# Performance work log

Measured on AMD Instinct MI355X. Metric: run time of the kernel, lower is better.

## Reference

```python
import jax, jax.numpy as jnp
import numpy as np

# ---- config (from repo's config module, standard values) ----
GH, GW = 32, 64            # control grid
FULL_H, FULL_W = 128, 512  # target_image (n_mels, frames)
N_FFT, HOP = 1024, 256
N_FREQ = N_FFT // 2 + 1    # 513
N_ITER, MOMENTUM = 32, 0.99
NUM_SAMPLES = 131072
BATCH = 8

# periodic hann window (torch.hann_window default)
_WIN = 0.5 * (1.0 - jnp.cos(2.0 * jnp.pi * jnp.arange(N_FFT) / N_FFT))


def _stft(x):
    # x: (B, L) -> (B, N_FREQ, F); center=True reflect pad, hann window
    pad = N_FFT // 2
    xp = jnp.pad(x, ((0, 0), (pad, pad)), mode='reflect')
    n_frames = 1 + (xp.shape[-1] - N_FFT) // HOP
    idx = jnp.arange(n_frames)[:, None] * HOP + jnp.arange(N_FFT)[None, :]
    frames = xp[:, idx] * _WIN  # (B, F, N_FFT)
    return jnp.fft.rfft(frames, axis=-1).transpose(0, 2, 1)  # (B, N_FREQ, F)


def _istft(S, length):
    # S: (B, N_FREQ, F) -> (B, length); windowed overlap-add, center trim
    frames = jnp.fft.irfft(S.transpose(0, 2, 1), n=N_FFT, axis=-1) * _WIN  # (B,F,N_FFT)
    B, F, _ = frames.shape
    total = N_FFT + HOP * (F - 1)
    idx = (jnp.arange(F)[:, None] * HOP + jnp.arange(N_FFT)[None, :]).reshape(-1)
    sig = jnp.zeros((B, total), frames.dtype).at[:, idx].add(frames.reshape(B, -1))
    wsq = jnp.zeros((total,), frames.dtype).at[idx].add(jnp.tile(_WIN ** 2, F))
    sig = sig / jnp.where(wsq > 1e-11, wsq, 1.0)
    pad = N_FFT // 2
    return sig[:, pad:pad + length]


def _griffin_lim(spec_power):
    # spec_power: (B, N_FREQ, W) power spectrogram (power=2.0)
    mag = jnp.sqrt(jnp.maximum(spec_power, 0.0))
    W = spec_power.shape[-1]
    length = HOP * (W - 1)
    # random unit-magnitude initial phase (torchaudio rand_init)
    u = jax.random.uniform(jax.random.key(1), mag.shape, dtype=jnp.float32)
    angles = jnp.exp(1j * (2.0 * jnp.pi) * u).astype(jnp.complex64)
    tprev = jnp.zeros_like(angles)
    for _ in range(N_ITER):  # fixed 32 iterations
        inverse = _istft(mag.astype(jnp.complex64) * angles, length)
        rebuilt = _stft(inverse)
        angles = rebuilt - tprev * (MOMENTUM / (1.0 + MOMENTUM))
        angles = angles / (jnp.abs(angles) + 1e-16)
        tprev = rebuilt
    return _istft(mag.astype(jnp.complex64) * angles, length)  # (B, length)


def setup_inputs() -> dict:
    key = jax.random.key(0)
    params = jax.random.uniform(key, (BATCH, GH * GW), dtype=jnp.float32)
    return {"params": params}


def reference(params):
    B = params.shape[0]
    grid = params.reshape(B, GH, GW)
    # F.interpolate(..., mode='bilinear', align_corners=False) == jax.image.resize bilinear
    full_spec = jax.image.resize(grid, (B, FULL_H, FULL_W), method='bilinear')  # (B,H,W)
    spec_power = full_spec ** 2 * 100.0
    linear_spec = jax.image.resize(spec_power, (B, N_FREQ, FULL_W), method='bilinear')
    audio = _griffin_lim(linear_spec)  # (B, (W-1)*HOP)
    # pad/trim to NUM_SAMPLES
    L = audio.shape[-1]
    if L < NUM_SAMPLES:
        audio = jnp.pad(audio, ((0, 0), (0, NUM_SAMPLES - L)))
    else:
        audio = audio[:, :NUM_SAMPLES]
    max_val = jnp.maximum(jnp.max(jnp.abs(audio), axis=-1, keepdims=True), 1e-8)
    audio = audio / max_val * 0.9
    return audio, full_spec
```

## Files before the change

kernel.cpp:

```cpp
#include <hip/hip_runtime.h>

typedef unsigned int u32;

constexpr int BATCH = 8;
constexpr int GH = 32, GW = 64;
constexpr int FH = 128, FW = 512;
constexpr int NFFT = 1024;
constexpr int HOP = 256;
constexpr int NFREQ = 513;
constexpr int NW = 512;
constexpr int SIGLEN = HOP * (NW - 1);
constexpr int TOTAL_LEN = NFFT + HOP*(NW-1);
constexpr int NITER = 32;
constexpr int NSAMP = 131072;
constexpr int NMAG = BATCH * NW * NFREQ;

#define SL(i) ((i) + ((i) >> 3))
constexpr int WSL = 576;

#define WAVEFENCE() __builtin_amdgcn_wave_barrier()

__device__ __forceinline__ void tf_round(u32 &x0, u32 &x1, int r) {
  x0 += x1;
  x1 = (x1 << r) | (x1 >> (32 - r));
  x1 ^= x0;
}

__device__ __forceinline__ void threefry2(u32 c0, u32 c1, u32 &o0, u32 &o1) {
  const u32 k0 = 0u, k1 = 1u;
  const u32 k2 = 0x1BD11BDAu ^ k0 ^ k1;
  u32 x0 = c0 + k0, x1 = c1 + k1;
  tf_round(x0, x1, 13); tf_round(x0, x1, 15); tf_round(x0, x1, 26); tf_round(x0, x1, 6);
  x0 += k1; x1 += k2 + 1u;
  tf_round(x0, x1, 17); tf_round(x0, x1, 29); tf_round(x0, x1, 16); tf_round(x0, x1, 24);
  x0 += k2; x1 += k0 + 2u;
  tf_round(x0, x1, 13); tf_round(x0, x1, 15); tf_round(x0, x1, 26); tf_round(x0, x1, 6);
  x0 += k0; x1 += k1 + 3u;
  tf_round(x0, x1, 17); tf_round(x0, x1, 29); tf_round(x0, x1, 16); tf_round(x0, x1, 24);
  x0 += k1; x1 += k2 + 4u;
  tf_round(x0, x1, 13); tf_round(x0, x1, 15); tf_round(x0, x1, 26); tf_round(x0, x1, 6);
  x0 += k2; x1 += k0 + 5u;
  o0 = x0; o1 = x1;
}

__global__ __launch_bounds__(256) void k_init(float* __restrict__ win,
                                              float2* __restrict__ tw512f, double2* __restrict__ twh,
                                              float* __restrict__ wsq,
                                              float2* __restrict__ tprev)
{
  int idx = blockIdx.x * 256 + threadIdx.x;
  int stride = gridDim.x * 256;
  const double PI2 = 6.283185307179586476925286766559;
  for (int t = idx; t < NFFT; t += stride)
    win[t] = (float)(0.5 * (1.0 - cos(PI2 * (double)t / 1024.0)));
  for (int k = idx; k < 512; k += stride) {
    double th = -PI2 * (double)k / 512.0;
    tw512f[k] = make_float2((float)cos(th), (float)sin(th));
    double th2 = -PI2 * (double)k / 1024.0;
    double2 v2; v2.x = cos(th2); v2.y = sin(th2);
    twh[k] = v2;
  }
  for (int j = idx; j < TOTAL_LEN; j += stride) {
    int gmax = j >> 8; if (gmax > NW - 1) gmax = NW - 1;
    int gmin = (j >= NFFT) ? ((j - (NFFT - 1) + 255) >> 8) : 0;
    float acc = 0.f;
    for (int g = gmin; g <= gmax; ++g) {
      float w = (float)(0.5 * (1.0 - cos(PI2 * (double)(j - (g << 8)) / 1024.0)));
      acc = __fadd_rn(acc, __fmul_rn(w, w));
    }
    wsq[j] = acc;
  }
  for (int i = idx; i < NMAG; i += stride)
    tprev[i] = make_float2(0.f, 0.f);
}

__device__ __forceinline__ void lin_taps(float sf, int in, int &i0, int &i1, float &w0, float &w1)
{
  if (sf <= 0.0f)                  { i0 = 0;      i1 = 0;      w0 = 1.0f; w1 = 0.0f; return; }
  if (sf >= (float)(in - 1))       { i0 = in - 1; i1 = in - 1; w0 = 1.0f; w1 = 0.0f; return; }
  i0 = (int)sf; i1 = i0 + 1;
  float x0 = __fsub_rn(sf, (float)i0);
  float a0 = __fsub_rn(1.0f, x0);
  float S  = __fadd_rn(a0, x0);
  w0 = __fdiv_rn(a0, S);
  w1 = __fdiv_rn(x0, S);
}

__device__ __forceinline__ float sf_H1(int H) {
  return __fadd_rn(__fmul_rn(__fadd_rn((float)H, 0.5f), 0.25f), -0.5f);
}
__device__ __forceinline__ float sf_W1(int W) {
  return __fadd_rn(__fmul_rn(__fadd_rn((float)W, 0.5f), 0.125f), -0.5f);
}
__device__ __forceinline__ float sf_H2(int K) {
  const float inv32 = (float)(1.0 / 4.0078125);
  return __fadd_rn(__fmul_rn(__fadd_rn((float)K, 0.5f), inv32), -0.5f);
}

__device__ __forceinline__ float fs_at(const float* __restrict__ pb, int H, int W)
{
  int r0, r1; float u0, u1;
  lin_taps(sf_H1(H), GH, r0, r1, u0, u1);
  int c0, c1; float v0, v1;
  lin_taps(sf_W1(W), GW, c0, c1, v0, v1);
  float t0 = __fmaf_rn(u1, pb[r1 * GW + c0], __fmul_rn(u0, pb[r0 * GW + c0]));
  float t1 = __fmaf_rn(u1, pb[r1 * GW + c1], __fmul_rn(u0, pb[r0 * GW + c1]));
  return __fmaf_rn(v1, t1, __fmul_rn(v0, t0));
}

__global__ __launch_bounds__(256) void k_fullspec(const float* __restrict__ p, float* __restrict__ fs)
{
  int idx = blockIdx.x * 256 + threadIdx.x;
  if (idx >= BATCH * FH * FW) return;
  int b = idx >> 16;
  int h = (idx >> 9) & (FH - 1);
  int w = idx & (FW - 1);
  fs[idx] = fs_at(p + b * (GH * GW), h, w);
}

__global__ __launch_bounds__(256) void k_mag(const float* __restrict__ p, float* __restrict__ mag)
{
  int idx = blockIdx.x * 256 + threadIdx.x;
  if (idx >= NMAG) return;
  int b = idx / (NW * NFREQ);
  int rem = idx - b * (NW * NFREQ);
  int f = rem / NFREQ;
  int k = rem - f * NFREQ;
  const float* pb = p + b * (GH * GW);
  int h0, h1; float wa, wb;
  lin_taps(sf_H2(k), FH, h0, h1, wa, wb);
  float fs0 = fs_at(pb, h0, f);
  float fs1 = fs_at(pb, h1, f);
  float P0 = __fmul_rn(__fmul_rn(fs0, fs0), 100.0f);
  float P1 = __fmul_rn(__fmul_rn(fs1, fs1), 100.0f);
  float lin = __fmaf_rn(wb, P1, __fmul_rn(wa, P0));
  mag[idx] = __fsqrt_rn(fmaxf(lin, 0.0f));
}

__global__ __launch_bounds__(256) void k_phase(float2* __restrict__ ang)
{
  int idx = blockIdx.x * 256 + threadIdx.x;
  if (idx >= NMAG) return;
  int b = idx / (NW * NFREQ);
  int rem = idx - b * (NW * NFREQ);
  int f = rem / NFREQ;
  int k = rem - f * NFREQ;
  u32 cnt = (u32)(b * (NFREQ * NW) + k * NW + f);
  u32 w0, w1;
  threefry2(0u, cnt, w0, w1);
  u32 bits = w0 ^ w1;
  float u = __uint_as_float((bits >> 9) | 0x3f800000u) - 1.0f;
  float th = __fmul_rn((float)6.283185307179586, u);
  double thd = (double)th;
  ang[idx] = make_float2((float)cos(thd), (float)sin(thd));
}

__device__ __forceinline__ float2 cadd2(float2 a, float2 b){ return make_float2(a.x+b.x, a.y+b.y); }
__device__ __forceinline__ float2 csub2(float2 a, float2 b){ return make_float2(a.x-b.x, a.y-b.y); }

template<bool INV>
__device__ __forceinline__ float2 twmul(float2 a, float2 w)
{
  float wy = INV ? -w.y : w.y;
  return make_float2(a.x*w.x - a.y*wy, a.x*wy + a.y*w.x);
}

template<bool INV>
__device__ __forceinline__ void bfly8(float2 x0, float2 x1, float2 x2, float2 x3,
                                      float2 x4, float2 x5, float2 x6, float2 x7,
                                      float2 &Y0, float2 &Y1, float2 &Y2, float2 &Y3,
                                      float2 &Y4, float2 &Y5, float2 &Y6, float2 &Y7)
{
  const float c = 0.70710678118654752440f;
  float2 u0 = cadd2(x0,x4), u1 = cadd2(x1,x5), u2 = cadd2(x2,x6), u3 = cadd2(x3,x7);
  float2 d0 = csub2(x0,x4), d1 = csub2(x1,x5), d2 = csub2(x2,x6), d3 = csub2(x3,x7);
  float2 w1, w2, w3;
  if (!INV) {
    w1 = make_float2(c*(d1.x + d1.y), c*(d1.y - d1.x));
    w2 = make_float2(d2.y, -d2.x);
    w3 = make_float2(c*(d3.y - d3.x), -c*(d3.x + d3.y));
  } else {
    w1 = make_float2(c*(d1.x - d1.y), c*(d1.x + d1.y));
    w2 = make_float2(-d2.y, d2.x);
    w3 = make_float2(-c*(d3.x + d3.y), c*(d3.x - d3.y));
  }
  float2 s0 = cadd2(u0,u2), s1 = cadd2(u1,u3), s2 = csub2(u0,u2);
  float2 e13 = csub2(u1,u3);
  float2 s3 = INV ? make_float2(-e13.y, e13.x) : make_float2(e13.y, -e13.x);
  float2 r0 = cadd2(d0,w2), r1 = cadd2(w1,w3), r2 = csub2(d0,w2);
  float2 e57 = csub2(w1,w3);
  float2 r3 = INV ? make_float2(-e57.y, e57.x) : make_float2(e57.y, -e57.x);
  Y0 = cadd2(s0,s1); Y4 = csub2(s0,s1);
  Y2 = cadd2(s2,s3); Y6 = csub2(s2,s3);
  Y1 = cadd2(r0,r1); Y5 = csub2(r0,r1);
  Y3 = cadd2(r2,r3); Y7 = csub2(r2,r3);
}

template<bool INV>
__device__ __forceinline__ void stage0_regs(float2* __restrict__ A, const float2* __restrict__ tw, int t,
    float2 x0, float2 x1, float2 x2, float2 x3, float2 x4, float2 x5, float2 x6, float2 x7)
{
  float2 Y0,Y1,Y2,Y3,Y4,Y5,Y6,Y7;
  bfly8<INV>(x0,x1,x2,x3,x4,x5,x6,x7, Y0,Y1,Y2,Y3,Y4,Y5,Y6,Y7);
  int ob = 8 * t;
  A[SL(ob + 0)] = Y0;
  A[SL(ob + 1)] = twmul<INV>(Y1, tw[t]);
  A[SL(ob + 2)] = twmul<INV>(Y2, tw[2 * t]);
  A[SL(ob + 3)] = twmul<INV>(Y3, tw[3 * t]);
  A[SL(ob + 4)] = twmul<INV>(Y4, tw[4 * t]);
  A[SL(ob + 5)] = twmul<INV>(Y5, tw[5 * t]);
  A[SL(ob + 6)] = twmul<INV>(Y6, tw[6 * t]);
  A[SL(ob + 7)] = twmul<INV>(Y7, tw[7 * t]);
}

template<bool INV>
__device__ __forceinline__ void stage_mid(float2* __restrict__ A, const float2* __restrict__ tw, int t)
{
  float2 x0 = A[SL(t)],       x1 = A[SL(t + 64)],  x2 = A[SL(t + 128)], x3 = A[SL(t + 192)];
  float2 x4 = A[SL(t + 256)], x5 = A[SL(t + 320)], x6 = A[SL(t + 384)], x7 = A[SL(t + 448)];
  float2 Y0,Y1,Y2,Y3,Y4,Y5,Y6,Y7;
  bfly8<INV>(x0,x1,x2,x3,x4,x5,x6,x7, Y0,Y1,Y2,Y3,Y4,Y5,Y6,Y7);
  WAVEFENCE();
  int p = t >> 3, q = t & 7;
  int base = 8 * p;
  int ob = q + 64 * p;
  A[SL(ob)]      = Y0;
  A[SL(ob + 8)]  = twmul<INV>(Y1, tw[base]);
  A[SL(ob + 16)] = twmul<INV>(Y2, tw[2 * base]);
  A[SL(ob + 24)] = twmul<INV>(Y3, tw[3 * base]);
  A[SL(ob + 32)] = twmul<INV>(Y4, tw[4 * base]);
  A[SL(ob + 40)] = twmul<INV>(Y5, tw[5 * base]);
  A[SL(ob + 48)] = twmul<INV>(Y6, tw[6 * base]);
  A[SL(ob + 56)] = twmul<INV>(Y7, tw[7 * base]);
}

template<bool INV>
__device__ __forceinline__ void stage_last_lds(float2* __restrict__ A, int t)
{
  float2 x0 = A[SL(t)],       x1 = A[SL(t + 64)],  x2 = A[SL(t + 128)], x3 = A[SL(t + 192)];
  float2 x4 = A[SL(t + 256)], x5 = A[SL(t + 320)], x6 = A[SL(t + 384)], x7 = A[SL(t + 448)];
  float2 Y0,Y1,Y2,Y3,Y4,Y5,Y6,Y7;
  bfly8<INV>(x0,x1,x2,x3,x4,x5,x6,x7, Y0,Y1,Y2,Y3,Y4,Y5,Y6,Y7);
  WAVEFENCE();
  A[SL(t)]       = Y0; A[SL(t + 64)]  = Y1; A[SL(t + 128)] = Y2; A[SL(t + 192)] = Y3;
  A[SL(t + 256)] = Y4; A[SL(t + 320)] = Y5; A[SL(t + 384)] = Y6; A[SL(t + 448)] = Y7;
}

template<bool INV>
__device__ __forceinline__ void stage_last_regs(const float2* __restrict__ A, int t,
    float2 &Y0, float2 &Y1, float2 &Y2, float2 &Y3, float2 &Y4, float2 &Y5, float2 &Y6, float2 &Y7)
{
  float2 x0 = A[SL(t)],       x1 = A[SL(t + 64)],  x2 = A[SL(t + 128)], x3 = A[SL(t + 192)];
  float2 x4 = A[SL(t + 256)], x5 = A[SL(t + 320)], x6 = A[SL(t + 384)], x7 = A[SL(t + 448)];
  bfly8<INV>(x0,x1,x2,x3,x4,x5,x6,x7, Y0,Y1,Y2,Y3,Y4,Y5,Y6,Y7);
}

__device__ __forceinline__ void upd_bin(float2* __restrict__ prow, float2* __restrict__ A,
                                        int k, double rx, double ry, float cf)
{
  float rxf = (float)rx, ryf = (float)ry;
  float2 pv = prow[k];
  float ax = __fsub_rn(rxf, __fmul_rn(pv.x, cf));
  float ay = __fsub_rn(ryf, __fmul_rn(pv.y, cf));
  double dx = (double)ax, dy = (double)ay;
  float d = (float)sqrt(dx * dx + dy * dy);
  float d2 = __fadd_rn(d, 1e-16f);
  float inv = __fdiv_rn(1.0f, d2);
  int slot = (k == 512) ? (WSL - 1) : SL(k);
  A[slot] = make_float2(__fmul_rn(ax, inv), __fmul_rn(ay, inv));
  prow[k] = make_float2(rxf, ryf);
}

__global__ __launch_bounds__(256) void k_istft(const float* __restrict__ mag, const float2* __restrict__ ang,
                                               float* __restrict__ frames,
                                               const float2* __restrict__ tw512f,
                                               const double2* __restrict__ twh,
                                               const float* __restrict__ win)
{
  __shared__ float2 ldsA[4 * WSL];
  __shared__ float2 twl[512];
  int tid = threadIdx.x;
  for (int i = tid; i < 512; i += 256) twl[i] = tw512f[i];
  __syncthreads();

  int wv = tid >> 6;
  int t  = tid & 63;
  int bf = (blockIdx.x << 2) + wv;
  float2* A = ldsA + wv * WSL;
  const float*  mrow = mag + bf * NFREQ;
  const float2* arow = ang + bf * NFREQ;

  float2 z0, z1, z2, z3, z4, z5, z6, z7;
#define PACKG(j, zj) { \
    int k = t + 64 * j; \
    if (k == 0) { \
      float m1 = mrow[0];   float2 a1 = arow[0]; \
      float m2 = mrow[512]; float2 a2 = arow[512]; \
      float S1x = __fmul_rn(m1, a1.x); \
      float S2x = __fmul_rn(m2, a2.x); \
      zj = make_float2((float)(0.5 * ((double)S1x + (double)S2x)), \
                       (float)(0.5 * ((double)S1x - (double)S2x))); \
    } else { \
      int k2 = 512 - k; \
      float m1 = mrow[k];  float2 a1 = arow[k]; \
      float m2 = mrow[k2]; float2 a2 = arow[k2]; \
      float S1x = __fmul_rn(m1, a1.x), S1y = __fmul_rn(m1, a1.y); \
      float S2x = __fmul_rn(m2, a2.x), S2y = __fmul_rn(m2, a2.y); \
      double Xex = 0.5 * ((double)S1x + (double)S2x); \
      double Xey = 0.5 * ((double)S1y - (double)S2y); \
      double Dx  = 0.5 * ((double)S1x - (double)S2x); \
      double Dy  = 0.5 * ((double)S1y + (double)S2y); \
      double2 w = twh[k]; \
      double ux = w.x * Dx + w.y * Dy; \
      double uy = w.x * Dy - w.y * Dx; \
      zj = make_float2((float)(Xex - uy), (float)(Xey + ux)); \
    } }
  PACKG(0, z0) PACKG(1, z1) PACKG(2, z2) PACKG(3, z3)
  PACKG(4, z4) PACKG(5, z5) PACKG(6, z6) PACKG(7, z7)

  stage0_regs<true>(A, twl, t, z0, z1, z2, z3, z4, z5, z6, z7);
  WAVEFENCE();
  stage_mid<true>(A, twl, t);
  WAVEFENCE();
  float2 y0, y1, y2, y3, y4, y5, y6, y7;
  stage_last_regs<true>(A, t, y0, y1, y2, y3, y4, y5, y6, y7);

  const float sc = 1.0f / 512.0f;
  const float2* win2 = (const float2*)win;
  float2* frow2 = (float2*)(frames + bf * NFFT);
#define STOREF(k, yk) { int m = t + 64 * k; float2 wv2 = win2[m]; \
    frow2[m] = make_float2(__fmul_rn(__fmul_rn(yk.x, sc), wv2.x), \
                           __fmul_rn(__fmul_rn(yk.y, sc), wv2.y)); }
  STOREF(0, y0) STOREF(1, y1) STOREF(2, y2) STOREF(3, y3)
  STOREF(4, y4) STOREF(5, y5) STOREF(6, y6) STOREF(7, y7)
}

__device__ __forceinline__ float sig_sample(const float* __restrict__ fb, const float* __restrict__ wsq, int j)
{
  int gmax = j >> 8; if (gmax > NW - 1) gmax = NW - 1;
  int gmin = (j >= NFFT) ? ((j - (NFFT - 1) + 255) >> 8) : 0;
  float acc = 0.f;
  for (int g = gmin; g <= gmax; ++g)
    acc = __fadd_rn(acc, fb[g * NFFT + (j - (g << 8))]);
  float wv = wsq[j];
  return __fdiv_rn(acc, wv > 1e-11f ? wv : 1.0f);
}

__global__ __launch_bounds__(256) void k_sig(const float* __restrict__ frames, const float* __restrict__ wsq,
                                             float* __restrict__ xp)
{
  int idx = blockIdx.x * 256 + threadIdx.x;
  int b = idx / TOTAL_LEN;
  int j = idx - b * TOTAL_LEN;
  int n = j - 512;
  if (n < 0) n = -n;
  if (n >= SIGLEN) n = 2 * SIGLEN - 2 - n;
  xp[idx] = sig_sample(frames + b * (NW * NFFT), wsq, n + 512);
}

__global__ __launch_bounds__(256) void k_fused(const float* __restrict__ xp,
                                               const float* __restrict__ win,
                                               const float2* __restrict__ tw512f,
                                               const double2* __restrict__ twh,
                                               const float* __restrict__ mag,
                                               float2* __restrict__ tprev,
                                               float* __restrict__ frames)
{
  __shared__ float2 ldsA[4 * WSL];
  __shared__ float2 twl[512];
  int tid = threadIdx.x;
  for (int i = tid; i < 512; i += 256) twl[i] = tw512f[i];
  __syncthreads();

  int wv = tid >> 6;
  int t  = tid & 63;
  int bf = (blockIdx.x << 2) + wv;
  int b = bf >> 9;
  int f = bf & (NW - 1);
  float2* A = ldsA + wv * WSL;
  const float2* win2 = (const float2*)win;

  const float2* xrow2 = (const float2*)(xp + b * TOTAL_LEN + f * HOP);
  float2 x0, x1, x2, x3, x4, x5, x6, x7;
#define LOADX(j, xj) { float2 xv = xrow2[t + 64 * j]; float2 wv2 = win2[t + 64 * j]; \
    xj = make_float2(__fmul_rn(xv.x, wv2.x), __fmul_rn(xv.y, wv2.y)); }
  LOADX(0, x0) LOADX(1, x1) LOADX(2, x2) LOADX(3, x3)
  LOADX(4, x4) LOADX(5, x5) LOADX(6, x6) LOADX(7, x7)
  stage0_regs<false>(A, twl, t, x0, x1, x2, x3, x4, x5, x6, x7);
  WAVEFENCE();
  stage_mid<false>(A, twl, t);
  WAVEFENCE();
  stage_last_lds<false>(A, t);
  WAVEFENCE();

  float2* prow = tprev + bf * NFREQ;
  const float cf = (float)(0.99 / 1.99);
#pragma unroll
  for (int j = 0; j < 4; ++j) {
    int k = t + 64 * j;
    if (k == 0) {
      float2 Z0 = A[SL(0)];
      double rx0 = (double)Z0.x + (double)Z0.y;
      double rx5 = (double)Z0.x - (double)Z0.y;
      upd_bin(prow, A, 0,   rx0, 0.0, cf);
      upd_bin(prow, A, 512, rx5, 0.0, cf);
    } else {
      int kc = 512 - k;
      float2 Zk = A[SL(k)];
      float2 Zc = A[SL(kc)];
      double Xex = 0.5 * ((double)Zk.x + (double)Zc.x);
      double Xey = 0.5 * ((double)Zk.y - (double)Zc.y);
      double Gx  = 0.5 * ((double)Zk.x - (double)Zc.x);
      double Gy  = 0.5 * ((double)Zk.y + (double)Zc.y);
      double2 w = twh[k];
      double P = w.x * Gy + w.y * Gx;
      double Q = w.y * Gy - w.x * Gx;
      upd_bin(prow, A, k,  Xex + P, Xey + Q, cf);
      upd_bin(prow, A, kc, Xex - P, Q - Xey, cf);
    }
  }
  if (t == 0) {
    float2 Zk = A[SL(256)];
    double Xex = 0.5 * ((double)Zk.x + (double)Zk.x);
    double Gy  = 0.5 * ((double)Zk.y + (double)Zk.y);
    double2 w = twh[256];
    double P = w.x * Gy;
    double Q = w.y * Gy;
    upd_bin(prow, A, 256, Xex + P, Q, cf);
  }
  WAVEFENCE();

  const float* mrow = mag + bf * NFREQ;
  float2 z0, z1, z2, z3, z4, z5, z6, z7;
#define PACKL(j, zj) { \
    int k = t + 64 * j; \
    if (k == 0) { \
      float m1 = mrow[0];   float2 a1 = A[SL(0)]; \
      float m2 = mrow[512]; float2 a2 = A[WSL - 1]; \
      float S1x = __fmul_rn(m1, a1.x); \
      float S2x = __fmul_rn(m2, a2.x); \
      zj = make_float2((float)(0.5 * ((double)S1x + (double)S2x)), \
                       (float)(0.5 * ((double)S1x - (double)S2x))); \
    } else { \
      int k2 = 512 - k; \
      float m1 = mrow[k];  float2 a1 = A[SL(k)]; \
      float m2 = mrow[k2]; float2 a2 = A[SL(k2)]; \
      float S1x = __fmul_rn(m1, a1.x), S1y = __fmul_rn(m1, a1.y); \
      float S2x = __fmul_rn(m2, a2.x), S2y = __fmul_rn(m2, a2.y); \
      double Xex = 0.5 * ((double)S1x + (double)S2x); \
      double Xey = 0.5 * ((double)S1y - (double)S2y); \
      double Dx  = 0.5 * ((double)S1x - (double)S2x); \
      double Dy  = 0.5 * ((double)S1y + (double)S2y); \
      double2 w = twh[k]; \
      double ux = w.x * Dx + w.y * Dy; \
      double uy = w.x * Dy - w.y * Dx; \
      zj = make_float2((float)(Xex - uy), (float)(Xey + ux)); \
    } }
  PACKL(0, z0) PACKL(1, z1) PACKL(2, z2) PACKL(3, z3)
  PACKL(4, z4) PACKL(5, z5) PACKL(6, z6) PACKL(7, z7)
  WAVEFENCE();

  stage0_regs<true>(A, twl, t, z0, z1, z2, z3, z4, z5, z6, z7);
  WAVEFENCE();
  stage_mid<true>(A, twl, t);
  WAVEFENCE();
  float2 y0, y1, y2, y3, y4, y5, y6, y7;
  stage_last_regs<true>(A, t, y0, y1, y2, y3, y4, y5, y6, y7);

  const float sc = 1.0f / 512.0f;
  float2* frow2 = (float2*)(frames + bf * NFFT);
  STOREF(0, y0) STOREF(1, y1) STOREF(2, y2) STOREF(3, y3)
  STOREF(4, y4) STOREF(5, y5) STOREF(6, y6) STOREF(7, y7)
}

__global__ __launch_bounds__(256) void k_ola(const float* __restrict__ frames, const float* __restrict__ wsq,
                                             float* __restrict__ audio, float* __restrict__ partial)
{
  int idx = blockIdx.x * 256 + threadIdx.x;
  int b  = idx >> 17;
  int nn = idx & (NSAMP - 1);
  float v = 0.f;
  if (nn < SIGLEN)
    v = sig_sample(frames + b * (NW * NFFT), wsq, nn + 512);
  audio[idx] = v;
  __shared__ float red[256];
  red[threadIdx.x] = fabsf(v);
  __syncthreads();
  for (int s = 128; s > 0; s >>= 1) {
    if (threadIdx.x < s) red[threadIdx.x] = fmaxf(red[threadIdx.x], red[threadIdx.x + s]);
    __syncthreads();
  }
  if (threadIdx.x == 0) partial[blockIdx.x] = red[0];
}

constexpr int OLA_BLK_PER_B = NSAMP / 256;

__global__ __launch_bounds__(256) void k_max2(const float* __restrict__ partial, float* __restrict__ maxbuf)
{
  int b = blockIdx.x;
  float m = 0.f;
  for (int i = threadIdx.x; i < OLA_BLK_PER_B; i += 256)
    m = fmaxf(m, partial[b * OLA_BLK_PER_B + i]);
  __shared__ float red[256];
  red[threadIdx.x] = m;
  __syncthreads();
  for (int s = 128; s > 0; s >>= 1) {
    if (threadIdx.x < s) red[threadIdx.x] = fmaxf(red[threadIdx.x], red[threadIdx.x + s]);
    __syncthreads();
  }
  if (threadIdx.x == 0) maxbuf[b] = red[0];
}

__global__ __launch_bounds__(256) void k_norm(const float* __restrict__ audio, const float* __restrict__ maxbuf,
                                              float* __restrict__ out)
{
  int idx = blockIdx.x * 256 + threadIdx.x;
  int b = idx >> 17;
  float m = fmaxf(maxbuf[b], 1e-8f);
  out[idx] = __fmul_rn(__fdiv_rn(audio[idx], m), 0.9f);
}

extern "C" void kernel_launch(void* const* d_in, const int* in_sizes, int n_in,
                              void* d_out, int out_size, void* d_ws, size_t ws_size,
                              hipStream_t stream)
{
  const float* params = (const float*)d_in[0];
  float* out   = (float*)d_out;
  float* audio_out = out;
  float* fs        = out + BATCH * NSAMP;

  float2*  tw512f = (float2*)d_ws;
  double2* twh    = (double2*)(tw512f + 512);
  float2*  ang    = (float2*)(twh + 512);
  float2*  tprev  = ang + NMAG;
  float*   frames = (float*)(tprev + NMAG);
  float*   mag    = frames + BATCH * NW * NFFT;
  float*   xp     = mag + NMAG;
  float*   win    = xp + BATCH * TOTAL_LEN;
  float*   wsq    = win + NFFT;
  float*   audio32= wsq + TOTAL_LEN;
  float*   maxbuf = audio32 + BATCH * NSAMP;
  float*   partial= maxbuf + BATCH;

  k_init<<<512, 256, 0, stream>>>(win, tw512f, twh, wsq, tprev);
  k_fullspec<<<(BATCH * FH * FW) / 256, 256, 0, stream>>>(params, fs);
  k_mag<<<(NMAG + 255) / 256, 256, 0, stream>>>(params, mag);
  k_phase<<<(NMAG + 255) / 256, 256, 0, stream>>>(ang);

  k_istft<<<BATCH * NW / 4, 256, 0, stream>>>(mag, (const float2*)ang, frames, tw512f, twh, win);
  for (int it = 0; it < NITER; ++it) {
    k_sig<<<(BATCH * TOTAL_LEN) / 256, 256, 0, stream>>>(frames, wsq, xp);
    k_fused<<<BATCH * NW / 4, 256, 0, stream>>>(xp, win, tw512f, twh, mag, tprev, frames);
  }
  k_ola<<<(BATCH * NSAMP) / 256, 256, 0, stream>>>(frames, wsq, audio32, partial);
  k_max2<<<BATCH, 256, 0, stream>>>(partial, maxbuf);
  k_norm<<<(BATCH * NSAMP) / 256, 256, 0, stream>>>(audio32, maxbuf, audio_out);
}
```

Baseline: 923.7 us.

## Fuse overlap-add signal reconstruction into the STFT kernel with ping-pong frame buffers

Removes the separate k_sig launch per iteration. Each fused block now rebuilds its needed span of the padded signal (4 frames' worth, 1792 samples) from the previous frames directly into LDS. The frame buffers are double-buffered, reusing the angle buffer, to avoid read/write races. This saves a kernel launch and the global round trip of xp per iteration. In exchange, overlapping samples are recomputed across blocks (about 1.75x redundancy) and the LDS footprint grows, which may lower occupancy.

```diff
diff --git a/kernel.cpp b/kernel.cpp
--- a/kernel.cpp
+++ b/kernel.cpp
@@ -17,6 +17,7 @@
 
 #define SL(i) ((i) + ((i) >> 3))
 constexpr int WSL = 576;
+constexpr int XSPAN = 4 * HOP + (NFFT - HOP);
 
 #define WAVEFENCE() __builtin_amdgcn_wave_barrier()
 
@@ -346,41 +347,45 @@
   return __fdiv_rn(acc, wv > 1e-11f ? wv : 1.0f);
 }
 
-__global__ __launch_bounds__(256) void k_sig(const float* __restrict__ frames, const float* __restrict__ wsq,
-                                             float* __restrict__ xp)
-{
-  int idx = blockIdx.x * 256 + threadIdx.x;
-  int b = idx / TOTAL_LEN;
-  int j = idx - b * TOTAL_LEN;
-  int n = j - 512;
-  if (n < 0) n = -n;
-  if (n >= SIGLEN) n = 2 * SIGLEN - 2 - n;
-  xp[idx] = sig_sample(frames + b * (NW * NFFT), wsq, n + 512);
-}
-
-__global__ __launch_bounds__(256) void k_fused(const float* __restrict__ xp,
+__global__ __launch_bounds__(256) void k_fused(const float* __restrict__ frames_in,
+                                               const float* __restrict__ wsq,
                                                const float* __restrict__ win,
                                                const float2* __restrict__ tw512f,
                                                const double2* __restrict__ twh,
                                                const float* __restrict__ mag,
                                                float2* __restrict__ tprev,
-                                               float* __restrict__ frames)
+                                               float* __restrict__ frames_out)
 {
   __shared__ float2 ldsA[4 * WSL];
   __shared__ float2 twl[512];
+  __shared__ float2 xpL2[XSPAN / 2];
+  float* xpL = (float*)xpL2;
   int tid = threadIdx.x;
   for (int i = tid; i < 512; i += 256) twl[i] = tw512f[i];
+
+  int bf0 = blockIdx.x << 2;
+  int b  = bf0 >> 9;
+  int f0 = bf0 & (NW - 1);
+  const float* fb = frames_in + b * (NW * NFFT);
+  int xbase = f0 * HOP;
+#pragma unroll
+  for (int c = 0; c < XSPAN / 256; ++c) {
+    int s = tid + 256 * c;
+    int j = xbase + s;
+    int n = j - 512;
+    if (n < 0) n = -n;
+    if (n >= SIGLEN) n = 2 * SIGLEN - 2 - n;
+    xpL[s] = sig_sample(fb, wsq, n + 512);
+  }
   __syncthreads();
 
   int wv = tid >> 6;
   int t  = tid & 63;
-  int bf = (blockIdx.x << 2) + wv;
-  int b = bf >> 9;
-  int f = bf & (NW - 1);
+  int bf = bf0 + wv;
   float2* A = ldsA + wv * WSL;
   const float2* win2 = (const float2*)win;
 
-  const float2* xrow2 = (const float2*)(xp + b * TOTAL_LEN + f * HOP);
+  const float2* xrow2 = (const float2*)(xpL + wv * HOP);
   float2 x0, x1, x2, x3, x4, x5, x6, x7;
 #define LOADX(j, xj) { float2 xv = xrow2[t + 64 * j]; float2 wv2 = win2[t + 64 * j]; \
     xj = make_float2(__fmul_rn(xv.x, wv2.x), __fmul_rn(xv.y, wv2.y)); }
@@ -468,7 +473,7 @@
   stage_last_regs<true>(A, t, y0, y1, y2, y3, y4, y5, y6, y7);
 
   const float sc = 1.0f / 512.0f;
-  float2* frow2 = (float2*)(frames + bf * NFFT);
+  float2* frow2 = (float2*)(frames_out + bf * NFFT);
   STOREF(0, y0) STOREF(1, y1) STOREF(2, y2) STOREF(3, y3)
   STOREF(4, y4) STOREF(5, y5) STOREF(6, y6) STOREF(7, y7)
 }
@@ -533,26 +538,28 @@
   double2* twh    = (double2*)(tw512f + 512);
   float2*  ang    = (float2*)(twh + 512);
   float2*  tprev  = ang + NMAG;
-  float*   frames = (float*)(tprev + NMAG);
-  float*   mag    = frames + BATCH * NW * NFFT;
-  float*   xp     = mag + NMAG;
-  float*   win    = xp + BATCH * TOTAL_LEN;
+  float*   framesA= (float*)(tprev + NMAG);
+  float*   mag    = framesA + BATCH * NW * NFFT;
+  float*   win    = mag + NMAG;
   float*   wsq    = win + NFFT;
   float*   audio32= wsq + TOTAL_LEN;
   float*   maxbuf = audio32 + BATCH * NSAMP;
   float*   partial= maxbuf + BATCH;
+  float*   framesB= (float*)ang;
 
   k_init<<<512, 256, 0, stream>>>(win, tw512f, twh, wsq, tprev);
   k_fullspec<<<(BATCH * FH * FW) / 256, 256, 0, stream>>>(params, fs);
   k_mag<<<(NMAG + 255) / 256, 256, 0, stream>>>(params, mag);
   k_phase<<<(NMAG + 255) / 256, 256, 0, stream>>>(ang);
 
-  k_istft<<<BATCH * NW / 4, 256, 0, stream>>>(mag, (const float2*)ang, frames, tw512f, twh, win);
+  k_istft<<<BATCH * NW / 4, 256, 0, stream>>>(mag, (const float2*)ang, framesA, tw512f, twh, win);
+  float* fin  = framesA;
+  float* fout = framesB;
   for (int it = 0; it < NITER; ++it) {
-    k_sig<<<(BATCH * TOTAL_LEN) / 256, 256, 0, stream>>>(frames, wsq, xp);
-    k_fused<<<BATCH * NW / 4, 256, 0, stream>>>(xp, win, tw512f, twh, mag, tprev, frames);
-  }
-  k_ola<<<(BATCH * NSAMP) / 256, 256, 0, stream>>>(frames, wsq, audio32, partial);
+    k_fused<<<BATCH * NW / 4, 256, 0, stream>>>(fin, wsq, win, tw512f, twh, mag, tprev, fout);
+    float* tmp = fin; fin = fout; fout = tmp;
+  }
+  k_ola<<<(BATCH * NSAMP) / 256, 256, 0, stream>>>(fin, wsq, audio32, partial);
   k_max2<<<BATCH, 256, 0, stream>>>(partial, maxbuf);
   k_norm<<<(BATCH * NSAMP) / 256, 256, 0, stream>>>(audio32, maxbuf, audio_out);
 }
```

Result: no change. 926.8 us (+0.3%).
